# Optimization experiments

Measured on AMD Instinct MI355X. Metric: run time of the kernel, lower is better.

The kernel has to match this reference:

```python
import jax, jax.numpy as jnp
import numpy as np

N, F_IN, HID, C = 50000, 256, 64, 40
E = 1_600_000
EPS = 1e-8  # torch cosine_similarity eps


def setup_inputs() -> dict:
    key = jax.random.key(0)
    ks = jax.random.split(key, 6)
    x = jax.random.normal(ks[0], (N, F_IN), jnp.float32)
    edge_index = jax.random.randint(ks[1], (2, E), 0, N, dtype=jnp.int64)
    edge_weights = jax.random.uniform(ks[2], (E,), jnp.float32)
    W1 = jax.random.normal(ks[3], (F_IN, HID), jnp.float32) / np.float32(np.sqrt(F_IN))
    b1 = jnp.zeros((HID,), jnp.float32)
    W2 = jax.random.normal(ks[4], (HID, C), jnp.float32) / np.float32(np.sqrt(HID))
    b2 = jnp.zeros((C,), jnp.float32)
    return {"x": x, "edge_index": edge_index, "edge_weights": edge_weights,
            "W1": W1, "b1": b1, "W2": W2, "b2": b2}


def _gcn_conv(x, W, b, src, dst, n):
    # PyG GCNConv: out = D^{-1/2} (A + I) D^{-1/2} (X W) + b
    xw = x @ W  # [n, out]
    loops = jnp.arange(n, dtype=src.dtype)
    s = jnp.concatenate([src, loops])  # self-loops appended
    d = jnp.concatenate([dst, loops])
    deg = jax.ops.segment_sum(jnp.ones_like(s, dtype=xw.dtype), d, num_segments=n)
    dinv = jnp.where(deg > 0, jax.lax.rsqrt(jnp.maximum(deg, 1.0)), 0.0)
    norm = dinv[s] * dinv[d]  # [E+n]
    msg = xw[s] * norm[:, None]  # gather + scale (irregular access)
    out = jax.ops.segment_sum(msg, d, num_segments=n)  # scatter-add
    return out + b


def reference(x, edge_index, edge_weights, W1, b1, W2, b2):
    src, dst = edge_index[0], edge_index[1]
    n = x.shape[0]
    # layer 1 + relu (dropout = identity in eval)
    h = jax.nn.relu(_gcn_conv(x, W1, b1, src, dst, n))
    x_out = _gcn_conv(h, W2, b2, src, dst, n)  # [n, C]
    # edge-wise cosine dissimilarity: 1 - cos(x_out[src], x_out[dst])
    a = x_out[src]
    b = x_out[dst]
    na = jnp.maximum(jnp.sqrt(jnp.sum(a * a, axis=-1)), EPS)
    nb = jnp.maximum(jnp.sqrt(jnp.sum(b * b, axis=-1)), EPS)
    cosine_sim = 1.0 - jnp.sum(a * b, axis=-1) / (na * nb)
    gnn_edge = jnp.where(edge_weights > 0.5, 1.0, -1.0)
    return (jax.nn.log_softmax(x_out, axis=1), x_out, cosine_sim, gnn_edge,
            jax.nn.softmax(x_out, axis=1))
```

## Files before the change

kernel.cpp:

```cpp
#include <hip/hip_runtime.h>
#include <hip/hip_bf16.h>

#define F_IN 256
#define HID  64
#define CLS  40
#define EPS  1e-8f
#define XS_STRIDE 264
#define H2_STRIDE 72
#define EPB  8192

typedef unsigned short ushort_t;
typedef unsigned int   uint_t;
typedef __attribute__((ext_vector_type(8))) short bf16x8;
typedef __attribute__((ext_vector_type(4))) float f32x4;

__device__ __forceinline__ float bf2f(ushort_t u) {
    union { uint_t i; float f; } v; v.i = ((uint_t)u) << 16; return v.f;
}
__device__ __forceinline__ ushort_t f2bf(float f) {
    union { float f; uint_t i; } v; v.f = f;
    uint_t r = v.i + 0x7fff + ((v.i >> 16) & 1);
    return (ushort_t)(r >> 16);
}
__device__ __forceinline__ float blo(uint_t p) {
    union { uint_t i; float f; } v; v.i = p << 16; return v.f;
}
__device__ __forceinline__ float bhi(uint_t p) {
    union { uint_t i; float f; } v; v.i = p & 0xffff0000u; return v.f;
}
__device__ __forceinline__ float dot_u4(uint4 a, uint4 b) {
    return blo(a.x) * blo(b.x) + bhi(a.x) * bhi(b.x)
         + blo(a.y) * blo(b.y) + bhi(a.y) * bhi(b.y)
         + blo(a.z) * blo(b.z) + bhi(a.z) * bhi(b.z)
         + blo(a.w) * blo(b.w) + bhi(a.w) * bhi(b.w);
}

__global__ void detect_kernel(const int* __restrict__ raw, int* __restrict__ flag) {
    int c = threadIdx.x;
    int w = raw[2 * c + 1];
    unsigned long long b = __ballot(w != 0);
    if (c == 0) *flag = (b == 0ULL) ? 1 : 0;
}

__global__ void build_hist_kernel(const void* __restrict__ raw, const int* __restrict__ flag,
                                  uint_t* __restrict__ pair, int* __restrict__ ghist, int E) {
    __shared__ int lhist[256];
    int tid = threadIdx.x;
    lhist[tid] = 0;
    __syncthreads();
    int base = blockIdx.x * EPB;
    if (*flag) {
        const long long* r = (const long long*)raw;
        for (int it = 0; it < EPB / 1024; ++it) {
            int e = base + (it * 256 + tid) * 4;
            if (e + 4 <= E) {
                ulonglong2 a0 = *(const ulonglong2*)(r + e);
                ulonglong2 a1 = *(const ulonglong2*)(r + e + 2);
                ulonglong2 b0 = *(const ulonglong2*)(r + E + e);
                ulonglong2 b1 = *(const ulonglong2*)(r + E + e + 2);
                uint_t d0 = (uint_t)b0.x, d1 = (uint_t)b0.y;
                uint_t d2 = (uint_t)b1.x, d3 = (uint_t)b1.y;
                uint4 p;
                p.x = (d0 << 16) | (uint_t)a0.x;
                p.y = (d1 << 16) | (uint_t)a0.y;
                p.z = (d2 << 16) | (uint_t)a1.x;
                p.w = (d3 << 16) | (uint_t)a1.y;
                *(uint4*)(pair + e) = p;
                atomicAdd(&lhist[d0 >> 8], 1);
                atomicAdd(&lhist[d1 >> 8], 1);
                atomicAdd(&lhist[d2 >> 8], 1);
                atomicAdd(&lhist[d3 >> 8], 1);
            } else {
                for (int k = 0; k < 4; ++k) {
                    int ee = e + k;
                    if (ee < E) {
                        uint_t s = (uint_t)r[ee];
                        uint_t d = (uint_t)r[E + ee];
                        pair[ee] = (d << 16) | s;
                        atomicAdd(&lhist[d >> 8], 1);
                    }
                }
            }
        }
    } else {
        const int* r = (const int*)raw;
        for (int it = 0; it < EPB / 1024; ++it) {
            int e = base + (it * 256 + tid) * 4;
            if (e + 4 <= E) {
                int4 a = *(const int4*)(r + e);
                int4 b = *(const int4*)(r + E + e);
                uint_t d0 = (uint_t)b.x, d1 = (uint_t)b.y;
                uint_t d2 = (uint_t)b.z, d3 = (uint_t)b.w;
                uint4 p;
                p.x = (d0 << 16) | (uint_t)a.x;
                p.y = (d1 << 16) | (uint_t)a.y;
                p.z = (d2 << 16) | (uint_t)a.z;
                p.w = (d3 << 16) | (uint_t)a.w;
                *(uint4*)(pair + e) = p;
                atomicAdd(&lhist[d0 >> 8], 1);
                atomicAdd(&lhist[d1 >> 8], 1);
                atomicAdd(&lhist[d2 >> 8], 1);
                atomicAdd(&lhist[d3 >> 8], 1);
            } else {
                for (int k = 0; k < 4; ++k) {
                    int ee = e + k;
                    if (ee < E) {
                        uint_t s = (uint_t)r[ee];
                        uint_t d = (uint_t)r[E + ee];
                        pair[ee] = (d << 16) | s;
                        atomicAdd(&lhist[d >> 8], 1);
                    }
                }
            }
        }
    }
    __syncthreads();
    ghist[blockIdx.x * 256 + tid] = lhist[tid];
}

__global__ void scan_cols_kernel(int* __restrict__ ghist, int* __restrict__ btot,
                                 int NBLK) {
    int k    = blockIdx.x;
    int lane = threadIdx.x;
    int carry = 0;
    for (int b0 = 0; b0 < NBLK; b0 += 64) {
        int b = b0 + lane;
        int v = (b < NBLK) ? ghist[b * 256 + k] : 0;
        int x = v;
        #pragma unroll
        for (int o = 1; o < 64; o <<= 1) {
            int t = __shfl_up(x, o);
            if (lane >= o) x += t;
        }
        if (b < NBLK) ghist[b * 256 + k] = carry + x - v;
        carry += __shfl(x, 63);
    }
    if (lane == 0) btot[k] = carry;
}

__global__ void scan_base_kernel(const int* __restrict__ btot, int* __restrict__ bbase) {
    __shared__ int s[256];
    int k = threadIdx.x;
    int v = btot[k];
    int x = v;
    s[k] = x;
    __syncthreads();
    #pragma unroll
    for (int o = 1; o < 256; o <<= 1) {
        int t = (k >= o) ? s[k - o] : 0;
        __syncthreads();
        x += t;
        s[k] = x;
        __syncthreads();
    }
    bbase[k] = x - v;
    if (k == 255) bbase[256] = x;
}

__global__ void scatter_buckets_kernel(const uint_t* __restrict__ pair,
                                       const int* __restrict__ ghist,
                                       const int* __restrict__ bbase,
                                       uint_t* __restrict__ bkt, int E) {
    __shared__ int cursor[256];
    int tid = threadIdx.x;
    cursor[tid] = ghist[blockIdx.x * 256 + tid] + bbase[tid];
    __syncthreads();
    int base = blockIdx.x * EPB;
    for (int it = 0; it < EPB / 256; ++it) {
        int e = base + it * 256 + tid;
        if (e < E) {
            uint_t u = pair[e];
            int pos = atomicAdd(&cursor[u >> 24], 1);
            bkt[pos] = u;
        }
    }
}

__global__ void bucket_csr_kernel(const uint_t* __restrict__ bkt,
                                  const int* __restrict__ bbase,
                                  ushort_t* __restrict__ csr, int* __restrict__ rowptr,
                                  float* __restrict__ dinv, int n, int E, int NBUCK) {
    __shared__ int lhist[256];
    __shared__ int lscan[256];
    __shared__ int cursor[256];
    int tid = threadIdx.x;
    int kb  = blockIdx.x;
    int base = bbase[kb];
    int cnt  = bbase[kb + 1] - base;
    lhist[tid] = 0;
    __syncthreads();
    for (int i = tid; i < cnt; i += 256) {
        uint_t u = bkt[base + i];
        atomicAdd(&lhist[(u >> 16) & 255], 1);
    }
    __syncthreads();
    int v = lhist[tid];
    int x = v;
    lscan[tid] = x;
    __syncthreads();
    #pragma unroll
    for (int o = 1; o < 256; o <<= 1) {
        int t = (tid >= o) ? lscan[tid - o] : 0;
        __syncthreads();
        x += t;
        lscan[tid] = x;
        __syncthreads();
    }
    int excl = x - v;
    int node = kb * 256 + tid;
    if (node < n) {
        rowptr[node] = base + excl;
        dinv[node]   = rsqrtf((float)(v + 1));
    }
    cursor[tid] = base + excl;
    if (kb == NBUCK - 1 && tid == 0) rowptr[n] = E;
    __syncthreads();
    for (int i = tid; i < cnt; i += 256) {
        uint_t u = bkt[base + i];
        int pos = atomicAdd(&cursor[(u >> 16) & 255], 1);
        csr[pos] = (ushort_t)(u & 0xffffu);
    }
}

__global__ void convert_w1_kernel(const float* __restrict__ W1, ushort_t* __restrict__ W1s) {
    int t = blockIdx.x * blockDim.x + threadIdx.x;
    if (t >= 4 * 8 * 64) return;
    int lane = t & 63;
    int kk   = (t >> 6) & 7;
    int nt   = t >> 9;
    int col  = nt * 16 + (lane & 15);
    int k0   = kk * 32 + (lane >> 4) * 8;
    ushort_t v[8];
    #pragma unroll
    for (int j = 0; j < 8; ++j) v[j] = f2bf(W1[(size_t)(k0 + j) * HID + col]);
    uint4 p;
    p.x = (uint_t)v[0] | ((uint_t)v[1] << 16);
    p.y = (uint_t)v[2] | ((uint_t)v[3] << 16);
    p.z = (uint_t)v[4] | ((uint_t)v[5] << 16);
    p.w = (uint_t)v[6] | ((uint_t)v[7] << 16);
    *(uint4*)(W1s + (size_t)t * 8) = p;
}

__global__ void convert_w2_kernel(const float* __restrict__ W2, ushort_t* __restrict__ W2s) {
    int t = blockIdx.x * blockDim.x + threadIdx.x;
    if (t >= 4 * 2 * 64) return;
    int lane = t & 63;
    int kk   = (t >> 6) & 1;
    int nt   = t >> 7;
    int col  = nt * 16 + (lane & 15);
    int k0   = kk * 32 + (lane >> 4) * 8;
    ushort_t v[8];
    #pragma unroll
    for (int j = 0; j < 8; ++j)
        v[j] = (col < CLS) ? f2bf(W2[(size_t)(k0 + j) * CLS + col]) : (ushort_t)0;
    uint4 p;
    p.x = (uint_t)v[0] | ((uint_t)v[1] << 16);
    p.y = (uint_t)v[2] | ((uint_t)v[3] << 16);
    p.z = (uint_t)v[4] | ((uint_t)v[5] << 16);
    p.w = (uint_t)v[6] | ((uint_t)v[7] << 16);
    *(uint4*)(W2s + (size_t)t * 8) = p;
}

__global__ void gemm1_mfma_kernel(const float* __restrict__ x,
                                  const ushort_t* __restrict__ W1s,
                                  const float* __restrict__ dinv,
                                  ushort_t* __restrict__ xws, int n) {
    __shared__ ushort_t xs[16 * XS_STRIDE];
    int node0 = blockIdx.x * 16;
    int tid = threadIdx.x;
    for (int i = tid; i < 16 * 64; i += 256) {
        int r  = i >> 6;
        int c4 = (i & 63) << 2;
        int node = node0 + r;
        float4 v = (node < n) ? *(const float4*)(x + (size_t)node * F_IN + c4)
                              : make_float4(0.f, 0.f, 0.f, 0.f);
        ushort4 b;
        b.x = f2bf(v.x); b.y = f2bf(v.y); b.z = f2bf(v.z); b.w = f2bf(v.w);
        *(ushort4*)(&xs[r * XS_STRIDE + c4]) = b;
    }
    __syncthreads();
    int wave = tid >> 6;
    int lane = tid & 63;
    int m    = lane & 15;
    int q    = lane >> 4;
    f32x4 acc = {0.f, 0.f, 0.f, 0.f};
    #pragma unroll
    for (int kk = 0; kk < 8; ++kk) {
        bf16x8 a = *(const bf16x8*)(&xs[m * XS_STRIDE + kk * 32 + q * 8]);
        bf16x8 b = *(const bf16x8*)(W1s + (((size_t)wave * 8 + kk) * 64 + lane) * 8);
        acc = __builtin_amdgcn_mfma_f32_16x16x32_bf16(a, b, acc, 0, 0, 0);
    }
    int ch = wave * 16 + m;
    #pragma unroll
    for (int r = 0; r < 4; ++r) {
        int node = node0 + q * 4 + r;
        if (node < n)
            xws[(size_t)node * HID + ch] = f2bf(acc[r] * dinv[node]);
    }
}

__global__ void gather1_kernel(const int* __restrict__ rowptr,
                               const ushort_t* __restrict__ csr,
                               const ushort_t* __restrict__ xws,
                               const float* __restrict__ dinv,
                               const float* __restrict__ b1,
                               ushort_t* __restrict__ h, int n) {
    int tid = threadIdx.x;
    int wv  = (blockIdx.x * blockDim.x + tid) >> 6;
    if (wv >= n) return;
    int l  = tid & 63;
    int g  = l >> 3;
    int lc = l & 7;
    int beg = rowptr[wv], endp = rowptr[wv + 1];
    float di = dinv[wv];
    float acc8[8];
    #pragma unroll
    for (int j = 0; j < 8; ++j) acc8[j] = 0.f;
    if (l < 8) {
        uint4 sv = *(const uint4*)(xws + (size_t)wv * HID + lc * 8);
        acc8[0] = blo(sv.x); acc8[1] = bhi(sv.x);
        acc8[2] = blo(sv.y); acc8[3] = bhi(sv.y);
        acc8[4] = blo(sv.z); acc8[5] = bhi(sv.z);
        acc8[6] = blo(sv.w); acc8[7] = bhi(sv.w);
    }
    for (int ch = beg; ch < endp; ch += 32) {
        #pragma unroll
        for (int k = 0; k < 4; ++k) {
            int e = ch + k * 8 + g;
            bool val = e < endp;
            int ec = val ? e : (endp - 1);
            int s = (int)csr[ec];
            uint4 p = *(const uint4*)(xws + (size_t)s * HID + lc * 8);
            if (!val) { p.x = 0u; p.y = 0u; p.z = 0u; p.w = 0u; }
            acc8[0] += blo(p.x); acc8[1] += bhi(p.x);
            acc8[2] += blo(p.y); acc8[3] += bhi(p.y);
            acc8[4] += blo(p.z); acc8[5] += bhi(p.z);
            acc8[6] += blo(p.w); acc8[7] += bhi(p.w);
        }
    }
    #pragma unroll
    for (int j = 0; j < 8; ++j) {
        float v = acc8[j];
        v += __shfl_xor(v, 8);
        v += __shfl_xor(v, 16);
        v += __shfl_xor(v, 32);
        acc8[j] = v;
    }
    if (l < 8) {
        float4 bb0 = *(const float4*)(b1 + lc * 8);
        float4 bb1 = *(const float4*)(b1 + lc * 8 + 4);
        float h0 = fmaxf(acc8[0] * di + bb0.x, 0.f);
        float h1 = fmaxf(acc8[1] * di + bb0.y, 0.f);
        float h2 = fmaxf(acc8[2] * di + bb0.z, 0.f);
        float h3 = fmaxf(acc8[3] * di + bb0.w, 0.f);
        float h4 = fmaxf(acc8[4] * di + bb1.x, 0.f);
        float h5 = fmaxf(acc8[5] * di + bb1.y, 0.f);
        float h6 = fmaxf(acc8[6] * di + bb1.z, 0.f);
        float h7 = fmaxf(acc8[7] * di + bb1.w, 0.f);
        uint4 pb;
        pb.x = (uint_t)f2bf(h0) | ((uint_t)f2bf(h1) << 16);
        pb.y = (uint_t)f2bf(h2) | ((uint_t)f2bf(h3) << 16);
        pb.z = (uint_t)f2bf(h4) | ((uint_t)f2bf(h5) << 16);
        pb.w = (uint_t)f2bf(h6) | ((uint_t)f2bf(h7) << 16);
        *(uint4*)(h + (size_t)wv * HID + lc * 8) = pb;
    }
}

__global__ void gemm2_mfma_kernel(const ushort_t* __restrict__ h,
                                  const ushort_t* __restrict__ W2s,
                                  const float* __restrict__ dinv,
                                  ushort_t* __restrict__ hws, int n) {
    __shared__ ushort_t hs[16 * H2_STRIDE];
    int node0 = blockIdx.x * 16;
    int tid = threadIdx.x;
    {
        int r  = tid >> 4;
        int c4 = (tid & 15) << 2;
        int node = node0 + r;
        ushort4 v = make_ushort4(0, 0, 0, 0);
        if (node < n) v = *(const ushort4*)(h + (size_t)node * HID + c4);
        *(ushort4*)(&hs[r * H2_STRIDE + c4]) = v;
    }
    __syncthreads();
    int wave = tid >> 6;
    int lane = tid & 63;
    int m    = lane & 15;
    int q    = lane >> 4;
    f32x4 acc = {0.f, 0.f, 0.f, 0.f};
    #pragma unroll
    for (int kk = 0; kk < 2; ++kk) {
        bf16x8 a = *(const bf16x8*)(&hs[m * H2_STRIDE + kk * 32 + q * 8]);
        bf16x8 b = *(const bf16x8*)(W2s + (((size_t)wave * 2 + kk) * 64 + lane) * 8);
        acc = __builtin_amdgcn_mfma_f32_16x16x32_bf16(a, b, acc, 0, 0, 0);
    }
    int ch = wave * 16 + m;
    #pragma unroll
    for (int r = 0; r < 4; ++r) {
        int node = node0 + q * 4 + r;
        if (node < n)
            hws[(size_t)node * HID + ch] = f2bf(acc[r] * dinv[node]);
    }
}

__global__ void gather2_fin_kernel(const int* __restrict__ rowptr,
                                   const ushort_t* __restrict__ csr,
                                   const ushort_t* __restrict__ hws,
                                   const float* __restrict__ dinv,
                                   const float* __restrict__ b2,
                                   float* __restrict__ xout, float* __restrict__ lsm,
                                   float* __restrict__ sm, ushort_t* __restrict__ xnb,
                                   int n) {
    int tid = threadIdx.x;
    int wv  = (blockIdx.x * blockDim.x + tid) >> 6;
    if (wv >= n) return;
    int l  = tid & 63;
    int g  = l >> 3;
    int lc = l & 7;
    int beg = rowptr[wv], endp = rowptr[wv + 1];
    float di = dinv[wv];
    float acc8[8];
    #pragma unroll
    for (int j = 0; j < 8; ++j) acc8[j] = 0.f;
    if (l < 8) {
        uint4 sv = *(const uint4*)(hws + (size_t)wv * HID + lc * 8);
        acc8[0] = blo(sv.x); acc8[1] = bhi(sv.x);
        acc8[2] = blo(sv.y); acc8[3] = bhi(sv.y);
        acc8[4] = blo(sv.z); acc8[5] = bhi(sv.z);
        acc8[6] = blo(sv.w); acc8[7] = bhi(sv.w);
    }
    for (int ch = beg; ch < endp; ch += 32) {
        #pragma unroll
        for (int k = 0; k < 4; ++k) {
            int e = ch + k * 8 + g;
            bool val = e < endp;
            int ec = val ? e : (endp - 1);
            int s = (int)csr[ec];
            uint4 p = *(const uint4*)(hws + (size_t)s * HID + lc * 8);
            if (!val) { p.x = 0u; p.y = 0u; p.z = 0u; p.w = 0u; }
            acc8[0] += blo(p.x); acc8[1] += bhi(p.x);
            acc8[2] += blo(p.y); acc8[3] += bhi(p.y);
            acc8[4] += blo(p.z); acc8[5] += bhi(p.z);
            acc8[6] += blo(p.w); acc8[7] += bhi(p.w);
        }
    }
    #pragma unroll
    for (int j = 0; j < 8; ++j) {
        float v = acc8[j];
        v += __shfl_xor(v, 8);
        v += __shfl_xor(v, 16);
        v += __shfl_xor(v, 32);
        acc8[j] = v;
    }
    bool cgv = lc < 5;
    float raw[8];
    if (cgv) {
        #pragma unroll
        for (int j = 0; j < 8; ++j) raw[j] = acc8[j] * di + b2[lc * 8 + j];
    } else {
        #pragma unroll
        for (int j = 0; j < 8; ++j) raw[j] = 0.f;
    }
    float mx = -3.0e38f;
    if (cgv) {
        #pragma unroll
        for (int j = 0; j < 8; ++j) mx = fmaxf(mx, raw[j]);
    }
    mx = fmaxf(mx, __shfl_xor(mx, 1));
    mx = fmaxf(mx, __shfl_xor(mx, 2));
    mx = fmaxf(mx, __shfl_xor(mx, 4));
    float ex[8];
    float ls = 0.f;
    if (cgv) {
        #pragma unroll
        for (int j = 0; j < 8; ++j) { ex[j] = __expf(raw[j] - mx); ls += ex[j]; }
    } else {
        #pragma unroll
        for (int j = 0; j < 8; ++j) ex[j] = 0.f;
    }
    ls += __shfl_xor(ls, 1);
    ls += __shfl_xor(ls, 2);
    ls += __shfl_xor(ls, 4);
    float sq = 0.f;
    if (cgv) {
        #pragma unroll
        for (int j = 0; j < 8; ++j) sq += raw[j] * raw[j];
    }
    sq += __shfl_xor(sq, 1);
    sq += __shfl_xor(sq, 2);
    sq += __shfl_xor(sq, 4);
    float rn = 1.0f / fmaxf(sqrtf(sq), EPS);
    if (l < 5) {
        size_t fb = (size_t)wv * CLS + l * 8;
        *(float4*)(xout + fb)     = make_float4(raw[0], raw[1], raw[2], raw[3]);
        *(float4*)(xout + fb + 4) = make_float4(raw[4], raw[5], raw[6], raw[7]);
        float lse = mx + __logf(ls);
        *(float4*)(lsm + fb)     = make_float4(raw[0] - lse, raw[1] - lse, raw[2] - lse, raw[3] - lse);
        *(float4*)(lsm + fb + 4) = make_float4(raw[4] - lse, raw[5] - lse, raw[6] - lse, raw[7] - lse);
        float inv = 1.0f / ls;
        *(float4*)(sm + fb)     = make_float4(ex[0] * inv, ex[1] * inv, ex[2] * inv, ex[3] * inv);
        *(float4*)(sm + fb + 4) = make_float4(ex[4] * inv, ex[5] * inv, ex[6] * inv, ex[7] * inv);
        uint4 pb;
        pb.x = (uint_t)f2bf(raw[0] * rn) | ((uint_t)f2bf(raw[1] * rn) << 16);
        pb.y = (uint_t)f2bf(raw[2] * rn) | ((uint_t)f2bf(raw[3] * rn) << 16);
        pb.z = (uint_t)f2bf(raw[4] * rn) | ((uint_t)f2bf(raw[5] * rn) << 16);
        pb.w = (uint_t)f2bf(raw[6] * rn) | ((uint_t)f2bf(raw[7] * rn) << 16);
        *(uint4*)(xnb + fb) = pb;
    }
}

__global__ void edge_kernel(const uint_t* __restrict__ pair,
                            const float* __restrict__ ew, const ushort_t* __restrict__ xnb,
                            float* __restrict__ cos_out, float* __restrict__ gnn_out, int E) {
    int tid = threadIdx.x;
    int wid = (blockIdx.x * blockDim.x + tid) >> 6;
    int l = tid & 63;
    int g = l >> 3;
    int j = l & 7;
    int e0 = wid * 32;
    if (e0 >= E) return;
    uint_t u[4];
    #pragma unroll
    for (int k = 0; k < 4; ++k) {
        int e = e0 + k * 8 + g;
        u[k] = (e < E) ? pair[e] : pair[E - 1];
    }
    uint4 av[4], bv[4];
    #pragma unroll
    for (int k = 0; k < 4; ++k) {
        int s = (int)(u[k] & 0xffffu);
        int d = (int)(u[k] >> 16);
        if (j < 5) {
            av[k] = *(const uint4*)(xnb + (size_t)s * CLS + j * 8);
            bv[k] = *(const uint4*)(xnb + (size_t)d * CLS + j * 8);
        }
    }
    #pragma unroll
    for (int k = 0; k < 4; ++k) {
        float part = 0.f;
        if (j < 5) part = dot_u4(av[k], bv[k]);
        part += __shfl_xor(part, 1);
        part += __shfl_xor(part, 2);
        part += __shfl_xor(part, 4);
        int e = e0 + k * 8 + g;
        if (j == 0 && e < E) {
            cos_out[e] = 1.0f - part;
            gnn_out[e] = (ew[e] > 0.5f) ? 1.0f : -1.0f;
        }
    }
}

extern "C" void kernel_launch(void* const* d_in, const int* in_sizes, int n_in,
                              void* d_out, int out_size, void* d_ws, size_t ws_size,
                              hipStream_t stream) {
    const float* x   = (const float*)d_in[0];
    const void*  ei  = d_in[1];
    const float* ew  = (const float*)d_in[2];
    const float* W1  = (const float*)d_in[3];
    const float* b1  = (const float*)d_in[4];
    const float* W2  = (const float*)d_in[5];
    const float* b2  = (const float*)d_in[6];

    const int n = in_sizes[0] / F_IN;
    const int E = in_sizes[2];

    float* lsm  = (float*)d_out;
    float* xout = lsm + (size_t)n * CLS;
    float* cosO = xout + (size_t)n * CLS;
    float* gnnO = cosO + E;
    float* smO  = gnnO + E;

    char* w = (char*)d_ws;
    auto alloc = [&](size_t bytes) {
        char* p = w;
        w += (bytes + 255) & ~(size_t)255;
        return p;
    };
    const int NBLK  = (E + EPB - 1) / EPB;
    const int NBUCK = (n + 255) / 256;

    uint_t*   pair   = (uint_t*)  alloc((size_t)E * 4);
    uint_t*   bkt    = (uint_t*)  alloc((size_t)E * 4);
    ushort_t* csr16  = (ushort_t*)alloc((size_t)E * 2);
    int*      ghist  = (int*)     alloc((size_t)NBLK * 256 * 4);
    int*      btot   = (int*)     alloc(256 * 4);
    int*      bbase  = (int*)     alloc(257 * 4);
    int*      rowptr = (int*)     alloc(((size_t)n + 1) * 4);
    float*    dinv   = (float*)   alloc((size_t)n * 4);
    ushort_t* xws    = (ushort_t*)alloc((size_t)n * HID * 2);
    ushort_t* hbuf   = (ushort_t*)alloc((size_t)n * HID * 2);
    ushort_t* hws    = (ushort_t*)alloc((size_t)n * HID * 2);
    ushort_t* xnb    = (ushort_t*)alloc((size_t)n * CLS * 2);
    ushort_t* W1s    = (ushort_t*)alloc((size_t)4 * 8 * 64 * 8 * 2);
    ushort_t* W2s    = (ushort_t*)alloc((size_t)4 * 2 * 64 * 8 * 2);
    int*      flag   = (int*)     alloc(64);

    detect_kernel<<<1, 64, 0, stream>>>((const int*)ei, flag);
    convert_w1_kernel<<<8, 256, 0, stream>>>(W1, W1s);
    convert_w2_kernel<<<2, 256, 0, stream>>>(W2, W2s);
    build_hist_kernel<<<NBLK, 256, 0, stream>>>(ei, flag, pair, ghist, E);
    scan_cols_kernel<<<256, 64, 0, stream>>>(ghist, btot, NBLK);
    scan_base_kernel<<<1, 256, 0, stream>>>(btot, bbase);
    scatter_buckets_kernel<<<NBLK, 256, 0, stream>>>(pair, ghist, bbase, bkt, E);
    bucket_csr_kernel<<<NBUCK, 256, 0, stream>>>(bkt, bbase, csr16, rowptr, dinv, n, E, NBUCK);
    gemm1_mfma_kernel<<<(n + 15) / 16, 256, 0, stream>>>(x, W1s, dinv, xws, n);
    gather1_kernel<<<((size_t)n * 64 + 255) / 256, 256, 0, stream>>>(rowptr, csr16, xws, dinv,
                                                                     b1, hbuf, n);
    gemm2_mfma_kernel<<<(n + 15) / 16, 256, 0, stream>>>(hbuf, W2s, dinv, hws, n);
    gather2_fin_kernel<<<((size_t)n * 64 + 255) / 256, 256, 0, stream>>>(rowptr, csr16, hws, dinv, b2,
                                                                         xout, lsm, smO, xnb, n);
    edge_kernel<<<((size_t)((E + 31) / 32) * 64 + 255) / 256, 256, 0, stream>>>(pair, ew, xnb, cosO, gnnO, E);
}
```

Before: 281.8 us.

## Compact layer-2 features to 40 channels, add nontemporal loads/stores, packed accumulation

Layer-2 projected features are stored with a stride of 40 instead of 64. This cuts the gather2 footprint and skips loads for the padded lanes. Index and output streams now use nontemporal loads and stores to avoid polluting the cache, and gather accumulation uses float2 vectors to encourage packed adds. Several unrelated tweaks are bundled together. The stride-40 rows start at 80-byte offsets, so the 16-byte vector loads stay aligned but rows no longer line up with cache lines.

```diff
diff --git a/kernel.cpp b/kernel.cpp
--- a/kernel.cpp
+++ b/kernel.cpp
@@ -13,6 +13,7 @@
 typedef unsigned int   uint_t;
 typedef __attribute__((ext_vector_type(8))) short bf16x8;
 typedef __attribute__((ext_vector_type(4))) float f32x4;
+typedef __attribute__((ext_vector_type(2))) float f32x2;
 
 __device__ __forceinline__ float bf2f(ushort_t u) {
     union { uint_t i; float f; } v; v.i = ((uint_t)u) << 16; return v.f;
@@ -27,6 +28,9 @@
 }
 __device__ __forceinline__ float bhi(uint_t p) {
     union { uint_t i; float f; } v; v.i = p & 0xffff0000u; return v.f;
+}
+__device__ __forceinline__ f32x2 unpk2(uint_t p) {
+    f32x2 r; r.x = blo(p); r.y = bhi(p); return r;
 }
 __device__ __forceinline__ float dot_u4(uint4 a, uint4 b) {
     return blo(a.x) * blo(b.x) + bhi(a.x) * bhi(b.x)
@@ -313,15 +317,11 @@
     int lc = l & 7;
     int beg = rowptr[wv], endp = rowptr[wv + 1];
     float di = dinv[wv];
-    float acc8[8];
-    #pragma unroll
-    for (int j = 0; j < 8; ++j) acc8[j] = 0.f;
+    f32x2 a01 = {0.f, 0.f}, a23 = {0.f, 0.f}, a45 = {0.f, 0.f}, a67 = {0.f, 0.f};
     if (l < 8) {
         uint4 sv = *(const uint4*)(xws + (size_t)wv * HID + lc * 8);
-        acc8[0] = blo(sv.x); acc8[1] = bhi(sv.x);
-        acc8[2] = blo(sv.y); acc8[3] = bhi(sv.y);
-        acc8[4] = blo(sv.z); acc8[5] = bhi(sv.z);
-        acc8[6] = blo(sv.w); acc8[7] = bhi(sv.w);
+        a01 += unpk2(sv.x); a23 += unpk2(sv.y);
+        a45 += unpk2(sv.z); a67 += unpk2(sv.w);
     }
     for (int ch = beg; ch < endp; ch += 32) {
         #pragma unroll
@@ -329,15 +329,14 @@
             int e = ch + k * 8 + g;
             bool val = e < endp;
             int ec = val ? e : (endp - 1);
-            int s = (int)csr[ec];
+            int s = (int)__builtin_nontemporal_load(csr + ec);
             uint4 p = *(const uint4*)(xws + (size_t)s * HID + lc * 8);
             if (!val) { p.x = 0u; p.y = 0u; p.z = 0u; p.w = 0u; }
-            acc8[0] += blo(p.x); acc8[1] += bhi(p.x);
-            acc8[2] += blo(p.y); acc8[3] += bhi(p.y);
-            acc8[4] += blo(p.z); acc8[5] += bhi(p.z);
-            acc8[6] += blo(p.w); acc8[7] += bhi(p.w);
-        }
-    }
+            a01 += unpk2(p.x); a23 += unpk2(p.y);
+            a45 += unpk2(p.z); a67 += unpk2(p.w);
+        }
+    }
+    float acc8[8] = {a01.x, a01.y, a23.x, a23.y, a45.x, a45.y, a67.x, a67.y};
     #pragma unroll
     for (int j = 0; j < 8; ++j) {
         float v = acc8[j];
@@ -394,11 +393,13 @@
         acc = __builtin_amdgcn_mfma_f32_16x16x32_bf16(a, b, acc, 0, 0, 0);
     }
     int ch = wave * 16 + m;
-    #pragma unroll
-    for (int r = 0; r < 4; ++r) {
-        int node = node0 + q * 4 + r;
-        if (node < n)
-            hws[(size_t)node * HID + ch] = f2bf(acc[r] * dinv[node]);
+    if (ch < CLS) {
+        #pragma unroll
+        for (int r = 0; r < 4; ++r) {
+            int node = node0 + q * 4 + r;
+            if (node < n)
+                hws[(size_t)node * CLS + ch] = f2bf(acc[r] * dinv[node]);
+        }
     }
 }
 
@@ -416,17 +417,14 @@
     int l  = tid & 63;
     int g  = l >> 3;
     int lc = l & 7;
+    bool chunk_ok = lc < 5;
     int beg = rowptr[wv], endp = rowptr[wv + 1];
     float di = dinv[wv];
-    float acc8[8];
-    #pragma unroll
-    for (int j = 0; j < 8; ++j) acc8[j] = 0.f;
-    if (l < 8) {
-        uint4 sv = *(const uint4*)(hws + (size_t)wv * HID + lc * 8);
-        acc8[0] = blo(sv.x); acc8[1] = bhi(sv.x);
-        acc8[2] = blo(sv.y); acc8[3] = bhi(sv.y);
-        acc8[4] = blo(sv.z); acc8[5] = bhi(sv.z);
-        acc8[6] = blo(sv.w); acc8[7] = bhi(sv.w);
+    f32x2 a01 = {0.f, 0.f}, a23 = {0.f, 0.f}, a45 = {0.f, 0.f}, a67 = {0.f, 0.f};
+    if (l < 5) {
+        uint4 sv = *(const uint4*)(hws + (size_t)wv * CLS + l * 8);
+        a01 += unpk2(sv.x); a23 += unpk2(sv.y);
+        a45 += unpk2(sv.z); a67 += unpk2(sv.w);
     }
     for (int ch = beg; ch < endp; ch += 32) {
         #pragma unroll
@@ -434,15 +432,15 @@
             int e = ch + k * 8 + g;
             bool val = e < endp;
             int ec = val ? e : (endp - 1);
-            int s = (int)csr[ec];
-            uint4 p = *(const uint4*)(hws + (size_t)s * HID + lc * 8);
-            if (!val) { p.x = 0u; p.y = 0u; p.z = 0u; p.w = 0u; }
-            acc8[0] += blo(p.x); acc8[1] += bhi(p.x);
-            acc8[2] += blo(p.y); acc8[3] += bhi(p.y);
-            acc8[4] += blo(p.z); acc8[5] += bhi(p.z);
-            acc8[6] += blo(p.w); acc8[7] += bhi(p.w);
-        }
-    }
+            int s = (int)__builtin_nontemporal_load(csr + ec);
+            uint4 p = make_uint4(0u, 0u, 0u, 0u);
+            if (val && chunk_ok)
+                p = *(const uint4*)(hws + (size_t)s * CLS + lc * 8);
+            a01 += unpk2(p.x); a23 += unpk2(p.y);
+            a45 += unpk2(p.z); a67 += unpk2(p.w);
+        }
+    }
+    float acc8[8] = {a01.x, a01.y, a23.x, a23.y, a45.x, a45.y, a67.x, a67.y};
     #pragma unroll
     for (int j = 0; j < 8; ++j) {
         float v = acc8[j];
@@ -451,7 +449,7 @@
         v += __shfl_xor(v, 32);
         acc8[j] = v;
     }
-    bool cgv = lc < 5;
+    bool cgv = chunk_ok;
     float raw[8];
     if (cgv) {
         #pragma unroll
@@ -491,14 +489,20 @@
     float rn = 1.0f / fmaxf(sqrtf(sq), EPS);
     if (l < 5) {
         size_t fb = (size_t)wv * CLS + l * 8;
-        *(float4*)(xout + fb)     = make_float4(raw[0], raw[1], raw[2], raw[3]);
-        *(float4*)(xout + fb + 4) = make_float4(raw[4], raw[5], raw[6], raw[7]);
+        f32x4 v0 = {raw[0], raw[1], raw[2], raw[3]};
+        f32x4 v1 = {raw[4], raw[5], raw[6], raw[7]};
+        __builtin_nontemporal_store(v0, (f32x4*)(xout + fb));
+        __builtin_nontemporal_store(v1, (f32x4*)(xout + fb + 4));
         float lse = mx + __logf(ls);
-        *(float4*)(lsm + fb)     = make_float4(raw[0] - lse, raw[1] - lse, raw[2] - lse, raw[3] - lse);
-        *(float4*)(lsm + fb + 4) = make_float4(raw[4] - lse, raw[5] - lse, raw[6] - lse, raw[7] - lse);
+        f32x4 l0 = {raw[0] - lse, raw[1] - lse, raw[2] - lse, raw[3] - lse};
+        f32x4 l1 = {raw[4] - lse, raw[5] - lse, raw[6] - lse, raw[7] - lse};
+        __builtin_nontemporal_store(l0, (f32x4*)(lsm + fb));
+        __builtin_nontemporal_store(l1, (f32x4*)(lsm + fb + 4));
         float inv = 1.0f / ls;
-        *(float4*)(sm + fb)     = make_float4(ex[0] * inv, ex[1] * inv, ex[2] * inv, ex[3] * inv);
-        *(float4*)(sm + fb + 4) = make_float4(ex[4] * inv, ex[5] * inv, ex[6] * inv, ex[7] * inv);
+        f32x4 s0 = {ex[0] * inv, ex[1] * inv, ex[2] * inv, ex[3] * inv};
+        f32x4 s1 = {ex[4] * inv, ex[5] * inv, ex[6] * inv, ex[7] * inv};
+        __builtin_nontemporal_store(s0, (f32x4*)(sm + fb));
+        __builtin_nontemporal_store(s1, (f32x4*)(sm + fb + 4));
         uint4 pb;
         pb.x = (uint_t)f2bf(raw[0] * rn) | ((uint_t)f2bf(raw[1] * rn) << 16);
         pb.y = (uint_t)f2bf(raw[2] * rn) | ((uint_t)f2bf(raw[3] * rn) << 16);
@@ -522,7 +526,8 @@
     #pragma unroll
     for (int k = 0; k < 4; ++k) {
         int e = e0 + k * 8 + g;
-        u[k] = (e < E) ? pair[e] : pair[E - 1];
+        int ec = (e < E) ? e : (E - 1);
+        u[k] = __builtin_nontemporal_load(pair + ec);
     }
     uint4 av[4], bv[4];
     #pragma unroll
@@ -543,8 +548,9 @@
         part += __shfl_xor(part, 4);
         int e = e0 + k * 8 + g;
         if (j == 0 && e < E) {
-            cos_out[e] = 1.0f - part;
-            gnn_out[e] = (ew[e] > 0.5f) ? 1.0f : -1.0f;
+            float w = __builtin_nontemporal_load(ew + e);
+            __builtin_nontemporal_store(1.0f - part, cos_out + e);
+            __builtin_nontemporal_store((w > 0.5f) ? 1.0f : -1.0f, gnn_out + e);
         }
     }
 }
@@ -588,7 +594,7 @@
     float*    dinv   = (float*)   alloc((size_t)n * 4);
     ushort_t* xws    = (ushort_t*)alloc((size_t)n * HID * 2);
     ushort_t* hbuf   = (ushort_t*)alloc((size_t)n * HID * 2);
-    ushort_t* hws    = (ushort_t*)alloc((size_t)n * HID * 2);
+    ushort_t* hws    = (ushort_t*)alloc((size_t)n * CLS * 2);
     ushort_t* xnb    = (ushort_t*)alloc((size_t)n * CLS * 2);
     ushort_t* W1s    = (ushort_t*)alloc((size_t)4 * 8 * 64 * 8 * 2);
     ushort_t* W2s    = (ushort_t*)alloc((size_t)4 * 2 * 64 * 8 * 2);
```

Result: slower. 293.9 us (+4.3%).
